# Kernel tuning notes

Hardware: AMD Instinct MI355X
Metric: run time of the kernel (lower is better)

The kernel has to match this reference:

```python
import jax, jax.numpy as jnp
import numpy as np


def setup_inputs() -> dict:
    key = jax.random.key(0)
    ks = jax.random.split(key, 4)
    B, T, D, U = 64, 2048, 256, 256
    x = jax.random.normal(ks[0], (B, T, D), dtype=jnp.float32)
    s = 1.0 / np.sqrt(D)
    kz = jax.random.normal(ks[1], (D, U), dtype=jnp.float32) * s
    kr = jax.random.normal(ks[2], (D, U), dtype=jnp.float32) * s
    kh = jax.random.normal(ks[3], (D, U), dtype=jnp.float32) * s
    return {
        'x': x, 'kz': kz, 'kr': kr, 'kh': kh,
        'mz': jnp.ones((U,), jnp.float32), 'mr': jnp.ones((U,), jnp.float32),
        'bz': jnp.zeros((U,), jnp.float32), 'br': jnp.zeros((U,), jnp.float32),
        'bh': jnp.zeros((U,), jnp.float32),
    }


def reference(x, kz, kr, kh, mz, mr, bz, br, bh):
    # Precompute the three input projections for all timesteps (batched GEMMs),
    # then scan the purely elementwise recurrence over time.
    xz = jnp.einsum('btd,du->btu', x, kz) + bz  # [B,T,U]
    xr = jnp.einsum('btd,du->btu', x, kr) + br
    xh = jnp.einsum('btd,du->btu', x, kh) + bh
    B, T, U = xz.shape
    h0 = jnp.zeros((B, U), x.dtype)

    def step(h, inp):
        xz_t, xr_t, xh_t = inp
        r = jnp.tanh(xr_t + h * mr) + 1.0
        z = jax.nn.sigmoid(xz_t + h * mz)
        hh = jnp.tanh(xh_t + r * h)
        out = (1.0 - z) * hh + z * h
        return out, out

    # scan over time axis: move T to leading axis
    xs = (jnp.swapaxes(xz, 0, 1), jnp.swapaxes(xr, 0, 1), jnp.swapaxes(xh, 0, 1))
    _, ys = jax.lax.scan(step, h0, xs)
    return jnp.swapaxes(ys, 0, 1)  # [B,T,U]
```

## Files before the change

kernel.cpp:

```cpp
#include <hip/hip_runtime.h>
#include <hip/hip_bf16.h>

#define BB 64
#define TT 2048
#define DD 256
#define UU 256
#define MM (BB*TT)
#define NN (3*UU)
#define PLANE ((size_t)BB*TT*UU)

typedef _Float16 half8 __attribute__((ext_vector_type(8)));
typedef _Float16 half4 __attribute__((ext_vector_type(4)));
typedef float floatx4 __attribute__((ext_vector_type(4)));

__device__ inline float fexp2(float x){
#if __has_builtin(__builtin_amdgcn_exp2f)
  return __builtin_amdgcn_exp2f(x);
#else
  return exp2f(x);
#endif
}
__device__ inline float frcp(float x){
#if __has_builtin(__builtin_amdgcn_rcpf)
  return __builtin_amdgcn_rcpf(x);
#else
  return 1.0f/x;
#endif
}
__device__ inline float ftanh(float a){
  const float TWO_L2E = 2.8853900817779268f;
  return 1.0f - 2.0f*frcp(fexp2(TWO_L2E*a) + 1.0f);
}
__device__ inline float fsigmoid(float a){
  const float L2E = 1.4426950408889634f;
  return frcp(1.0f + fexp2(-L2E*a));
}

__global__ __launch_bounds__(256) void prep_kernel(const float* __restrict__ kz,
                                                   const float* __restrict__ kr,
                                                   const float* __restrict__ kh,
                                                   _Float16* __restrict__ K16T){
  int o = blockIdx.x*256 + threadIdx.x;
  int n = o >> 8;
  int k = o & 255;
  int p = n >> 8;
  int u = n & 255;
  const float* w = (p==0) ? kz : ((p==1) ? kr : kh);
  K16T[o] = (_Float16)w[k*UU + u];
}

#define BM 128
#define BN 128
#define BK 32
#define AS_OFF 0
#define BS_OFF 4096
#define CT_LDT 136

__global__ __launch_bounds__(256) void gemm_kernel(const float* __restrict__ X,
                                                   const _Float16* __restrict__ K16T,
                                                   const float* __restrict__ bz,
                                                   const float* __restrict__ br,
                                                   const float* __restrict__ bh,
                                                   _Float16* __restrict__ P){
  __shared__ __align__(16) _Float16 smem[8704];
  const int tid = threadIdx.x;

  const int l   = blockIdx.y*6 + blockIdx.x;
  const int xcd = l & 7;
  const int idx = l >> 3;
  const int pnl = idx / 6;
  const int by  = xcd*128 + pnl;
  const int bx  = idx - pnl*6;
  const int rowBase = by*BM;
  const int nBase   = bx*BN;

  const int wave = tid >> 6, lane = tid & 63;
  const int wm = wave & 1, wn = wave >> 1;
  const int lrow = lane & 15, lkq = lane >> 4;

  floatx4 acc[4][4] = {};

  const int arow = tid & 127;
  const int asel = tid >> 7;
  const float* aptr = X + (size_t)(rowBase + arow)*DD + asel*16;
  _Float16* aw0 = smem + AS_OFF + ((asel*2 + 0)*128 + arow)*8;
  _Float16* aw1 = smem + AS_OFF + ((asel*2 + 1)*128 + arow)*8;

  const _Float16* bsrc = K16T + (size_t)(nBase + (tid & 127))*DD + (tid >> 7)*8;

  for (int k0 = 0; k0 < DD; k0 += BK) {
    __syncthreads();
    floatx4 a0 = *(const floatx4*)(aptr + k0);
    floatx4 a1 = *(const floatx4*)(aptr + k0 + 4);
    floatx4 a2 = *(const floatx4*)(aptr + k0 + 8);
    floatx4 a3 = *(const floatx4*)(aptr + k0 + 12);
    __builtin_amdgcn_global_load_lds(
        (const __attribute__((address_space(1))) void*)(bsrc + k0),
        (__attribute__((address_space(3))) void*)(smem + BS_OFF + tid*8),
        16, 0, 0);
    __builtin_amdgcn_global_load_lds(
        (const __attribute__((address_space(1))) void*)(bsrc + k0 + 16),
        (__attribute__((address_space(3))) void*)(smem + BS_OFF + (tid + 256)*8),
        16, 0, 0);
    half8 pk0, pk1;
    #pragma unroll
    for (int q = 0; q < 4; q++){
      pk0[q]   = (_Float16)a0[q];
      pk0[4+q] = (_Float16)a1[q];
      pk1[q]   = (_Float16)a2[q];
      pk1[4+q] = (_Float16)a3[q];
    }
    *(half8*)aw0 = pk0;
    *(half8*)aw1 = pk1;
    __syncthreads();
    half8 af[4], bf[4];
    #pragma unroll
    for (int i = 0; i < 4; i++)
      af[i] = *(const half8*)&smem[AS_OFF + (lkq*128 + wm*64 + i*16 + lrow)*8];
    #pragma unroll
    for (int j = 0; j < 4; j++)
      bf[j] = *(const half8*)&smem[BS_OFF + (lkq*128 + wn*64 + j*16 + lrow)*8];
    #pragma unroll
    for (int i = 0; i < 4; i++)
      #pragma unroll
      for (int j = 0; j < 4; j++)
        acc[i][j] = __builtin_amdgcn_mfma_f32_16x16x32_f16(af[i], bf[j], acc[i][j], 0, 0, 0);
  }

  const int p = bx >> 1;
  const int ub = (bx & 1) * 128;
  const float* bias = (p==0) ? bz : ((p==1) ? br : bh);
  _Float16* Pp = P + (size_t)p * PLANE;
  const int bidx  = rowBase >> 11;
  const int trow0 = rowBase & 2047;
  const int u_r = tid >> 2, tc = tid & 3;

  #pragma unroll
  for (int h = 0; h < 2; h++){
    __syncthreads();
    if (wn == h){
      #pragma unroll
      for (int j = 0; j < 4; j++){
        const int u_l = j*16 + lrow;
        const float bv = bias[ub + h*64 + u_l];
        #pragma unroll
        for (int i = 0; i < 4; i++){
          half4 v;
          #pragma unroll
          for (int r = 0; r < 4; r++)
            v[r] = (_Float16)(acc[i][j][r] + bv);
          *(half4*)&smem[u_l*CT_LDT + wm*64 + i*16 + lkq*4] = v;
        }
      }
    }
    __syncthreads();
    _Float16* dst = Pp + (size_t)(bidx*UU + ub + h*64 + u_r)*TT + trow0 + tc*32;
    const _Float16* srcp = smem + u_r*CT_LDT + tc*32;
    #pragma unroll
    for (int q = 0; q < 4; q++)
      *(half8*)(dst + q*8) = *(const half8*)(srcp + q*8);
  }
}

#define PF 16
#define NBUF 4
__global__ __launch_bounds__(64) void scan_kernel(const _Float16* __restrict__ P,
                                                  const float* __restrict__ mz,
                                                  const float* __restrict__ mr,
                                                  float* __restrict__ out){
  const int ci = blockIdx.x*64 + threadIdx.x;
  const int b = ci >> 8;
  const int u = ci & 255;
  const half8* pz = (const half8*)(P + (size_t)ci*TT);
  const half8* pr = (const half8*)(P + PLANE + (size_t)ci*TT);
  const half8* ph = (const half8*)(P + 2*PLANE + (size_t)ci*TT);
  float* po = out + (size_t)b*(TT*UU) + u;
  const float vmz = mz[u], vmr = mr[u];
  float h = 0.0f;

  half8 qz[NBUF][2], qr[NBUF][2], qh[NBUF][2];

#define LOADC(buf, c) do { \
    qz[buf][0] = pz[(c)*2];   qz[buf][1] = pz[(c)*2+1]; \
    qr[buf][0] = pr[(c)*2];   qr[buf][1] = pr[(c)*2+1]; \
    qh[buf][0] = ph[(c)*2];   qh[buf][1] = ph[(c)*2+1]; \
  } while(0)

#define PROC(buf, c) do { \
    _Pragma("unroll") \
    for (int i = 0; i < PF; i++){ \
      float xz = (float)qz[buf][i>>3][i&7]; \
      float xr = (float)qr[buf][i>>3][i&7]; \
      float xh = (float)qh[buf][i>>3][i&7]; \
      float r  = ftanh(xr + h*vmr) + 1.0f; \
      float z  = fsigmoid(xz + h*vmz); \
      float hh = ftanh(xh + r*h); \
      h = (1.0f - z)*hh + z*h; \
      po[(size_t)((c)*PF + i)*UU] = h; \
    } \
    if ((c) + NBUF < NC) LOADC(buf, (c) + NBUF); \
  } while(0)

  const int NC = TT/PF;
  LOADC(0, 0); LOADC(1, 1); LOADC(2, 2); LOADC(3, 3);
  for (int c = 0; c < NC; c += NBUF){
    PROC(0, c);
    PROC(1, c+1);
    PROC(2, c+2);
    PROC(3, c+3);
  }
#undef LOADC
#undef PROC
}

extern "C" void kernel_launch(void* const* d_in, const int* in_sizes, int n_in,
                              void* d_out, int out_size, void* d_ws, size_t ws_size,
                              hipStream_t stream) {
  (void)in_sizes; (void)n_in; (void)out_size; (void)ws_size;
  const float* x  = (const float*)d_in[0];
  const float* kz = (const float*)d_in[1];
  const float* kr = (const float*)d_in[2];
  const float* kh = (const float*)d_in[3];
  const float* mz = (const float*)d_in[4];
  const float* mr = (const float*)d_in[5];
  const float* bz = (const float*)d_in[6];
  const float* br = (const float*)d_in[7];
  const float* bh = (const float*)d_in[8];
  float* out = (float*)d_out;

  _Float16* K16T = (_Float16*)d_ws;
  _Float16* P    = (_Float16*)((char*)d_ws + 393216);

  hipLaunchKernelGGL(prep_kernel, dim3(NN*DD/256), dim3(256), 0, stream, kz, kr, kh, K16T);
  hipLaunchKernelGGL(gemm_kernel, dim3(NN/BN, MM/BM), dim3(256), 0, stream,
                     x, K16T, bz, br, bh, P);
  hipLaunchKernelGGL(scan_kernel, dim3(256), dim3(64), 0, stream, P, mz, mr, out);
}
```

Measured before the change: 524.0 us.

## Interleave two scan chains per thread and store GEMM epilogue directly

The scan kernel now gives each thread two independent recurrence chains (channels u and u+64) with interleaved transcendental work to hide dependency latency. It launches half as many blocks and halves the prefetch depth to bound register use. The GEMM epilogue drops the shared-memory transpose and writes half4 fragments straight to global memory, removing two barriers per half but making the stores narrower and less coalesced. On a 256-CU device, 128 single-wave blocks leave many CUs idle, trading parallelism for ILP.

```diff
diff --git a/kernel.cpp b/kernel.cpp
--- a/kernel.cpp
+++ b/kernel.cpp
@@ -54,7 +54,6 @@
 #define BK 32
 #define AS_OFF 0
 #define BS_OFF 4096
-#define CT_LDT 136
 
 __global__ __launch_bounds__(256) void gemm_kernel(const float* __restrict__ X,
                                                    const _Float16* __restrict__ K16T,
@@ -62,7 +61,7 @@
                                                    const float* __restrict__ br,
                                                    const float* __restrict__ bh,
                                                    _Float16* __restrict__ P){
-  __shared__ __align__(16) _Float16 smem[8704];
+  __shared__ __align__(16) _Float16 smem[8192];
   const int tid = threadIdx.x;
 
   const int l   = blockIdx.y*6 + blockIdx.x;
@@ -131,83 +130,88 @@
   const int ub = (bx & 1) * 128;
   const float* bias = (p==0) ? bz : ((p==1) ? br : bh);
   _Float16* Pp = P + (size_t)p * PLANE;
-  const int bidx  = rowBase >> 11;
-  const int trow0 = rowBase & 2047;
-  const int u_r = tid >> 2, tc = tid & 3;
-
+  const int bidx = rowBase >> 11;
+  const int t0 = (rowBase & 2047) + wm*64 + lkq*4;
   #pragma unroll
-  for (int h = 0; h < 2; h++){
-    __syncthreads();
-    if (wn == h){
+  for (int j = 0; j < 4; j++){
+    int col = ub + wn*64 + j*16 + lrow;
+    float bv = bias[col];
+    _Float16* rowp = Pp + (size_t)(bidx*UU + col)*TT + t0;
+    #pragma unroll
+    for (int i = 0; i < 4; i++){
+      half4 v;
       #pragma unroll
-      for (int j = 0; j < 4; j++){
-        const int u_l = j*16 + lrow;
-        const float bv = bias[ub + h*64 + u_l];
-        #pragma unroll
-        for (int i = 0; i < 4; i++){
-          half4 v;
-          #pragma unroll
-          for (int r = 0; r < 4; r++)
-            v[r] = (_Float16)(acc[i][j][r] + bv);
-          *(half4*)&smem[u_l*CT_LDT + wm*64 + i*16 + lkq*4] = v;
-        }
-      }
+      for (int r = 0; r < 4; r++)
+        v[r] = (_Float16)(acc[i][j][r] + bv);
+      *(half4*)(rowp + i*16) = v;
     }
-    __syncthreads();
-    _Float16* dst = Pp + (size_t)(bidx*UU + ub + h*64 + u_r)*TT + trow0 + tc*32;
-    const _Float16* srcp = smem + u_r*CT_LDT + tc*32;
-    #pragma unroll
-    for (int q = 0; q < 4; q++)
-      *(half8*)(dst + q*8) = *(const half8*)(srcp + q*8);
   }
 }
 
 #define PF 16
-#define NBUF 4
+#define NBUF 2
 __global__ __launch_bounds__(64) void scan_kernel(const _Float16* __restrict__ P,
                                                   const float* __restrict__ mz,
                                                   const float* __restrict__ mr,
                                                   float* __restrict__ out){
-  const int ci = blockIdx.x*64 + threadIdx.x;
-  const int b = ci >> 8;
-  const int u = ci & 255;
-  const half8* pz = (const half8*)(P + (size_t)ci*TT);
-  const half8* pr = (const half8*)(P + PLANE + (size_t)ci*TT);
-  const half8* ph = (const half8*)(P + 2*PLANE + (size_t)ci*TT);
-  float* po = out + (size_t)b*(TT*UU) + u;
-  const float vmz = mz[u], vmr = mr[u];
-  float h = 0.0f;
-
-  half8 qz[NBUF][2], qr[NBUF][2], qh[NBUF][2];
+  const int lid = threadIdx.x;
+  const int g   = blockIdx.x;
+  const int c0  = g*128 + lid;
+  const int c1  = c0 + 64;
+  const int b   = c0 >> 8;
+  const int u0  = c0 & 255;
+  const int u1  = u0 + 64;
+  const half8* pz0 = (const half8*)(P + (size_t)c0*TT);
+  const half8* pr0 = (const half8*)(P + PLANE + (size_t)c0*TT);
+  const half8* ph0 = (const half8*)(P + 2*PLANE + (size_t)c0*TT);
+  const half8* pz1 = (const half8*)(P + (size_t)c1*TT);
+  const half8* pr1 = (const half8*)(P + PLANE + (size_t)c1*TT);
+  const half8* ph1 = (const half8*)(P + 2*PLANE + (size_t)c1*TT);
+  float* po0 = out + (size_t)b*(TT*UU) + u0;
+  float* po1 = po0 + 64;
+  const float vmz0 = mz[u0], vmr0 = mr[u0];
+  const float vmz1 = mz[u1], vmr1 = mr[u1];
+  float h0 = 0.0f, h1 = 0.0f;
+
+  half8 qz[NBUF][2][2], qr[NBUF][2][2], qh[NBUF][2][2];
 
 #define LOADC(buf, c) do { \
-    qz[buf][0] = pz[(c)*2];   qz[buf][1] = pz[(c)*2+1]; \
-    qr[buf][0] = pr[(c)*2];   qr[buf][1] = pr[(c)*2+1]; \
-    qh[buf][0] = ph[(c)*2];   qh[buf][1] = ph[(c)*2+1]; \
+    qz[buf][0][0] = pz0[(c)*2]; qz[buf][0][1] = pz0[(c)*2+1]; \
+    qr[buf][0][0] = pr0[(c)*2]; qr[buf][0][1] = pr0[(c)*2+1]; \
+    qh[buf][0][0] = ph0[(c)*2]; qh[buf][0][1] = ph0[(c)*2+1]; \
+    qz[buf][1][0] = pz1[(c)*2]; qz[buf][1][1] = pz1[(c)*2+1]; \
+    qr[buf][1][0] = pr1[(c)*2]; qr[buf][1][1] = pr1[(c)*2+1]; \
+    qh[buf][1][0] = ph1[(c)*2]; qh[buf][1][1] = ph1[(c)*2+1]; \
   } while(0)
 
 #define PROC(buf, c) do { \
     _Pragma("unroll") \
     for (int i = 0; i < PF; i++){ \
-      float xz = (float)qz[buf][i>>3][i&7]; \
-      float xr = (float)qr[buf][i>>3][i&7]; \
-      float xh = (float)qh[buf][i>>3][i&7]; \
-      float r  = ftanh(xr + h*vmr) + 1.0f; \
-      float z  = fsigmoid(xz + h*vmz); \
-      float hh = ftanh(xh + r*h); \
-      h = (1.0f - z)*hh + z*h; \
-      po[(size_t)((c)*PF + i)*UU] = h; \
+      float xz0 = (float)qz[buf][0][i>>3][i&7]; \
+      float xr0 = (float)qr[buf][0][i>>3][i&7]; \
+      float xh0 = (float)qh[buf][0][i>>3][i&7]; \
+      float xz1 = (float)qz[buf][1][i>>3][i&7]; \
+      float xr1 = (float)qr[buf][1][i>>3][i&7]; \
+      float xh1 = (float)qh[buf][1][i>>3][i&7]; \
+      float r0  = ftanh(xr0 + h0*vmr0) + 1.0f; \
+      float r1  = ftanh(xr1 + h1*vmr1) + 1.0f; \
+      float z0  = fsigmoid(xz0 + h0*vmz0); \
+      float z1  = fsigmoid(xz1 + h1*vmz1); \
+      float hh0 = ftanh(xh0 + r0*h0); \
+      float hh1 = ftanh(xh1 + r1*h1); \
+      h0 = (1.0f - z0)*hh0 + z0*h0; \
+      h1 = (1.0f - z1)*hh1 + z1*h1; \
+      po0[(size_t)((c)*PF + i)*UU] = h0; \
+      po1[(size_t)((c)*PF + i)*UU] = h1; \
     } \
     if ((c) + NBUF < NC) LOADC(buf, (c) + NBUF); \
   } while(0)
 
   const int NC = TT/PF;
-  LOADC(0, 0); LOADC(1, 1); LOADC(2, 2); LOADC(3, 3);
+  LOADC(0, 0); LOADC(1, 1);
   for (int c = 0; c < NC; c += NBUF){
     PROC(0, c);
     PROC(1, c+1);
-    PROC(2, c+2);
-    PROC(3, c+3);
   }
 #undef LOADC
 #undef PROC
@@ -234,5 +238,5 @@
   hipLaunchKernelGGL(prep_kernel, dim3(NN*DD/256), dim3(256), 0, stream, kz, kr, kh, K16T);
   hipLaunchKernelGGL(gemm_kernel, dim3(NN/BN, MM/BM), dim3(256), 0, stream,
                      x, K16T, bz, br, bh, P);
-  hipLaunchKernelGGL(scan_kernel, dim3(256), dim3(64), 0, stream, P, mz, mr, out);
-}
+  hipLaunchKernelGGL(scan_kernel, dim3(128), dim3(64), 0, stream, P, mz, mr, out);
+}
```

After: 640.5 us. 1.22x slower.
